# Optimization experiments

Measured on AMD Instinct MI355X. Metric: run time of the kernel, lower is better.

The kernel has to match this reference:

```python
import jax, jax.numpy as jnp
import numpy as np

B, D, L = 8, 512, 8192


def log_g(x):
    # th.where(x >= 0, log(relu(x) + 1), x)
    return jnp.where(x >= 0, jnp.log1p(jnp.maximum(x, 0.0)), x)


def min_gru(hg):
    # hg: [B, H, L] -> [B, H/2, L]
    h, gate = jnp.split(hg, 2, axis=1)
    log_coeffs = -jax.nn.softplus(gate)                      # log a_t
    log_values = -jax.nn.softplus(-gate) + log_g(h)          # log b_t
    a_star = jnp.cumsum(log_coeffs, axis=2)
    log_h0_plus_b_star = jax.lax.cumlogsumexp(log_values - a_star, axis=2)
    return jnp.exp(a_star + log_h0_plus_b_star)


def conv1x1(x, w, b):
    # x: [B, D, L], w: [E, D], b: [E]  (kernel-size-1 Conv1d == pointwise linear)
    return jnp.einsum('ed,bdl->bel', w, x) + b[None, :, None]


def setup_inputs() -> dict:
    key = jax.random.key(0)
    k1, k2, k3, k4, k5 = jax.random.split(key, 5)
    scale = 1.0 / np.sqrt(D)
    x = jax.random.normal(k1, (B, D, L), dtype=jnp.float32)
    w_fore = jax.random.normal(k2, (D, D), dtype=jnp.float32) * scale
    b_fore = jax.random.normal(k3, (D,), dtype=jnp.float32) * scale
    w_back = jax.random.normal(k4, (D, D), dtype=jnp.float32) * scale
    b_back = jax.random.normal(k5, (D,), dtype=jnp.float32) * scale
    return {'x': x, 'w_fore': w_fore, 'b_fore': b_fore, 'w_back': w_back, 'b_back': b_back}


def reference(x, w_fore, b_fore, w_back, b_back):
    fore = min_gru(conv1x1(x, w_fore, b_fore))                            # [B, D/2, L]
    back = jnp.flip(min_gru(conv1x1(jnp.flip(x, 2), w_back, b_back)), 2)  # [B, D/2, L]
    return jnp.concatenate([fore, back], axis=1)                          # [B, D, L]
```

## Files before the change

kernel.cpp:

```cpp
#include <hip/hip_runtime.h>

#define BATCH 8
#define DIN   512
#define SEQ   8192
#define ECH   1024
#define HCH   256
#define CL    32
#define NCHNK (SEQ / CL)
#define NSC   16

typedef __bf16 bf16;
typedef __bf16 bf16x8 __attribute__((ext_vector_type(8)));
typedef float  floatx4 __attribute__((ext_vector_type(4)));

__device__ __forceinline__ void async_ld16(void* lds, const void* g) {
  __builtin_amdgcn_global_load_lds(
      (const __attribute__((address_space(1))) unsigned int*)g,
      (__attribute__((address_space(3))) unsigned int*)lds, 16, 0, 0);
}

__device__ __forceinline__ float bits2f(unsigned u) {
  return __builtin_bit_cast(float, u);
}

__device__ __forceinline__ void gru_ab(unsigned v, float& a, float& bt) {
  float hh = bits2f(v << 16);
  float g  = bits2f(v & 0xffff0000u);
  float eg = __expf(-g);
  float sg = 1.f / (1.f + eg);
  a = eg * sg;
  float gv = hh >= 0.f ? 1.f + hh : __expf(hh);
  bt = sg * gv;
}

__global__ void k_wconv(const float* __restrict__ wf, const float* __restrict__ bfo,
                        const float* __restrict__ wb, const float* __restrict__ bb,
                        bf16* __restrict__ Wf, float* __restrict__ bias) {
  int idx = blockIdx.x * 256 + threadIdx.x;
  if (idx < ECH * DIN) {
    int n = idx >> 9, d = idx & 511;
    int dir = n >> 9, r = n & 511, e = r >> 1, isg = r & 1;
    int s = e + (isg ? HCH : 0);
    const float* w = dir ? wb : wf;
    size_t o = ((size_t)((n >> 4) * 16 + (d >> 5)) << 9) +
               ((((d >> 3) & 3) * 16 + (n & 15)) << 3) + (d & 7);
    Wf[o] = (bf16)w[s * DIN + d];
  }
  if (idx < ECH) {
    int dir = idx >> 9, r = idx & 511, e = r >> 1, isg = r & 1;
    int s = e + (isg ? HCH : 0);
    bias[idx] = (dir ? bb : bfo)[s];
  }
}

__global__ void k_xpose(const float* __restrict__ x, bf16* __restrict__ xT) {
  __shared__ float T[64 * 65];
  int t = threadIdx.x;
  int l0 = blockIdx.x * 64;
  int d0 = blockIdx.y * 64;
  int b  = blockIdx.z;
  const float* xb = x + (size_t)b * DIN * SEQ;
#pragma unroll
  for (int p = 0; p < 4; ++p) {
    int dl = (t >> 4) + p * 16;
    int l4 = (t & 15) * 4;
    float4 v = *(const float4*)(xb + (size_t)(d0 + dl) * SEQ + l0 + l4);
    T[dl * 65 + l4 + 0] = v.x;
    T[dl * 65 + l4 + 1] = v.y;
    T[dl * 65 + l4 + 2] = v.z;
    T[dl * 65 + l4 + 3] = v.w;
  }
  __syncthreads();
  bf16* xTb = xT + (size_t)b * SEQ * DIN;
#pragma unroll
  for (int p = 0; p < 2; ++p) {
    int ll = (t >> 3) + p * 32;
    int d8 = (t & 7) * 8;
    bf16x8 h;
#pragma unroll
    for (int j = 0; j < 8; ++j) h[j] = (bf16)T[(d8 + j) * 65 + ll];
    *(bf16x8*)(xTb + (size_t)(l0 + ll) * DIN + d0 + d8) = h;
  }
}

#define BKK 64
#define NKT (DIN / BKK)

__launch_bounds__(256, 3)
__global__ void k_gemm(const bf16* __restrict__ xT, const bf16* __restrict__ Wf,
                       const float* __restrict__ bias, bf16* __restrict__ hg,
                       float* __restrict__ Asum, float* __restrict__ Bsum) {
  __shared__ __align__(16) bf16 lds[16896];
  bf16* As = lds;

  int t = threadIdx.x;
  int lane = t & 63, wave = t >> 6;
  int l15 = lane & 15, quad = lane >> 4, rsw = l15 & 7;
  int wm = wave >> 1, wn = wave & 1;
  int mb = wm * 64, nb = wn * 64;

  int lin = blockIdx.x + 8 * blockIdx.y;
  int xcd = lin & 7;
  int seq = lin >> 3;
  int ltile = xcd + 8 * (seq >> 3);
  int ntile = seq & 7;
  int n0 = ntile * 128;
  int l0 = ltile * 128;
  int b  = blockIdx.z;

  const bf16* gA = xT + ((size_t)b * SEQ + l0) * DIN;
  int nb16 = (n0 >> 4) + wn * 4;

  float bb4[4];
#pragma unroll
  for (int ni = 0; ni < 4; ++ni) bb4[ni] = bias[n0 + nb + ni * 16 + l15];

  int srow = wave * 32 + (lane >> 3);
  int scol = ((lane & 7) ^ ((lane >> 3) & 7)) * 8;

  floatx4 acc[4][4];
#pragma unroll
  for (int i = 0; i < 4; ++i)
#pragma unroll
    for (int j = 0; j < 4; ++j) acc[i][j] = (floatx4){0.f, 0.f, 0.f, 0.f};

#pragma unroll
  for (int kt = 0; kt < NKT; ++kt) {
    int k0 = kt * BKK;
#pragma unroll
    for (int q = 0; q < 4; ++q)
      async_ld16(As + (wave * 32 + q * 8) * 64,
                 gA + (size_t)(srow + q * 8) * DIN + k0 + scol);

    bf16x8 bfr[4][2];
#pragma unroll
    for (int i = 0; i < 4; ++i)
#pragma unroll
      for (int k2 = 0; k2 < 2; ++k2)
        bfr[i][k2] = *(const bf16x8*)(Wf +
            (((size_t)(nb16 + i) * 16 + kt * 2 + k2) << 9) + lane * 8);

    __syncthreads();

#pragma unroll
    for (int k2 = 0; k2 < 2; ++k2) {
      bf16x8 af[4];
#pragma unroll
      for (int i = 0; i < 4; ++i)
        af[i] = *(const bf16x8*)(As + (mb + i * 16 + l15) * 64 +
                                 (((k2 * 4 + quad) ^ rsw) * 8));
#pragma unroll
      for (int mi = 0; mi < 4; ++mi)
#pragma unroll
        for (int ni = 0; ni < 4; ++ni)
          acc[mi][ni] = __builtin_amdgcn_mfma_f32_16x16x32_bf16(
              af[mi], bfr[ni][k2], acc[mi][ni], 0, 0, 0);
    }
    __syncthreads();
  }

  bf16* Cs = lds;
#pragma unroll
  for (int mi = 0; mi < 4; ++mi)
#pragma unroll
    for (int ni = 0; ni < 4; ++ni)
#pragma unroll
      for (int r = 0; r < 4; ++r) {
        int row = mb + mi * 16 + quad * 4 + r;
        int col = nb + ni * 16 + l15;
        Cs[row * 132 + col] = (bf16)(acc[mi][ni][r] + bb4[ni]);
      }
  __syncthreads();
  bf16* hgb = hg + ((size_t)b * SEQ + l0) * ECH + n0;
#pragma unroll
  for (int p = 0; p < 8; ++p) {
    int row = p * 16 + (t >> 4);
    int seg = t & 15;
    *(bf16x8*)(hgb + (size_t)row * ECH + seg * 8) =
        *(const bf16x8*)(Cs + row * 132 + seg * 8);
  }

  {
    int dirn = ntile >> 2;
    int c = wave, el = lane;
    float A = 1.f, Bc = 0.f;
#pragma unroll 8
    for (int i = 0; i < CL; ++i) {
      int row = c * CL + (dirn ? (CL - 1 - i) : i);
      unsigned v = *(const unsigned*)(Cs + row * 132 + 2 * el);
      float a, bt;
      gru_ab(v, a, bt);
      A *= a;
      Bc = a * Bc + bt;
    }
    int chunkg = ltile * 4 + c;
    int eg = ((n0 & 511) >> 1) + el;
    size_t o = ((size_t)(b * 2 + dirn) * NCHNK + chunkg) * 256 + eg;
    Asum[o] = A;
    Bsum[o] = Bc;
  }
}

__global__ void k_scan2(const float* __restrict__ Asum, const float* __restrict__ Bsum,
                        float* __restrict__ hin) {
  int e = threadIdx.x, row2 = blockIdx.x, dir = row2 & 1;
  size_t base = (size_t)row2 * NCHNK;
  float h = 0.f;
#pragma unroll 8
  for (int i = 0; i < NCHNK; ++i) {
    int c = dir ? (NCHNK - 1 - i) : i;
    size_t o = (base + c) * 256 + e;
    hin[o] = h;
    h = Asum[o] * h + Bsum[o];
  }
}

__global__ void k_scan3(const bf16* __restrict__ hg, const float* __restrict__ hin,
                        float* __restrict__ out) {
  __shared__ float T[256 * 33];
  int t = threadIdx.x;
  int chunk = blockIdx.x, dir = blockIdx.y, b = blockIdx.z;
  const bf16* hb = hg + (size_t)b * SEQ * ECH + dir * 512 + 2 * t;
  float h = hin[((size_t)(b * 2 + dir) * NCHNK + chunk) * 256 + t];
  int lbase = chunk * CL;
#pragma unroll 8
  for (int i = 0; i < CL; ++i) {
    int ll = dir ? (CL - 1 - i) : i;
    unsigned v = *(const unsigned*)(hb + (size_t)(lbase + ll) * ECH);
    float a, bt;
    gru_ab(v, a, bt);
    h = a * h + bt;
    T[t * 33 + ll] = h;
  }
  __syncthreads();
  float* ob = out + ((size_t)b * 512 + dir * 256) * SEQ + lbase;
#pragma unroll
  for (int p = 0; p < 8; ++p) {
    int row = p * 32 + (t >> 3);
    int c4 = (t & 7) * 4;
    float4 v4;
    v4.x = T[row * 33 + c4 + 0];
    v4.y = T[row * 33 + c4 + 1];
    v4.z = T[row * 33 + c4 + 2];
    v4.w = T[row * 33 + c4 + 3];
    *(float4*)(ob + (size_t)row * SEQ + c4) = v4;
  }
}

extern "C" void kernel_launch(void* const* d_in, const int* in_sizes, int n_in,
                              void* d_out, int out_size, void* d_ws, size_t ws_size,
                              hipStream_t stream) {
  const float* x   = (const float*)d_in[0];
  const float* wf  = (const float*)d_in[1];
  const float* bfo = (const float*)d_in[2];
  const float* wb  = (const float*)d_in[3];
  const float* bb  = (const float*)d_in[4];
  float* out = (float*)d_out;
  char* ws = (char*)d_ws;

  bf16*  xT   = (bf16*)(ws);
  bf16*  hg   = (bf16*)(ws + 67108864);
  bf16*  Wfm  = (bf16*)(ws + 201326592);
  float* bias = (float*)(ws + 202375168);
  float* Asum = (float*)(ws + 202379264);
  float* Bsum = (float*)(ws + 206573568);
  float* hin  = (float*)(ws + 210767872);

  k_wconv<<<2048, 256, 0, stream>>>(wf, bfo, wb, bb, Wfm, bias);
  k_xpose<<<dim3(SEQ / 64, DIN / 64, BATCH), 256, 0, stream>>>(x, xT);
  k_gemm<<<dim3(ECH / 128, SEQ / 128, BATCH), 256, 0, stream>>>(xT, Wfm, bias, hg,
                                                                Asum, Bsum);
  k_scan2<<<16, 256, 0, stream>>>(Asum, Bsum, hin);
  k_scan3<<<dim3(NCHNK, 2, BATCH), 256, 0, stream>>>(hg, hin, out);
}
```

Baseline: 382.9 us.

## Store per-step prefix (A,B) pairs from GEMM and split the chunk carry scan hierarchically

The GEMM epilogue now writes packed bf16 prefix products A and prefix affine offsets B for every timestep in place of the raw h/gate tensor, laid out in scan order. The final pass then computes each output as a*h0+b without recomputing exps or running a serial recurrence. The single 16-block serial carry scan over 256 chunks becomes a three-level scan (per-superchunk reduce, 16-step scan, expand) to expose more parallelism. Rounding the prefix products to bf16 loses precision, and the epilogue now issues strided 4-byte global stores per timestep.

```diff
diff --git a/kernel.cpp b/kernel.cpp
--- a/kernel.cpp
+++ b/kernel.cpp
@@ -88,7 +88,7 @@
 
 __launch_bounds__(256, 3)
 __global__ void k_gemm(const bf16* __restrict__ xT, const bf16* __restrict__ Wf,
-                       const float* __restrict__ bias, bf16* __restrict__ hg,
+                       const float* __restrict__ bias, unsigned* __restrict__ P,
                        float* __restrict__ Asum, float* __restrict__ Bsum) {
   __shared__ __align__(16) bf16 lds[16896];
   bf16* As = lds;
@@ -171,66 +171,91 @@
         Cs[row * 132 + col] = (bf16)(acc[mi][ni][r] + bb4[ni]);
       }
   __syncthreads();
-  bf16* hgb = hg + ((size_t)b * SEQ + l0) * ECH + n0;
-#pragma unroll
-  for (int p = 0; p < 8; ++p) {
-    int row = p * 16 + (t >> 4);
-    int seg = t & 15;
-    *(bf16x8*)(hgb + (size_t)row * ECH + seg * 8) =
-        *(const bf16x8*)(Cs + row * 132 + seg * 8);
-  }
 
   {
     int dirn = ntile >> 2;
     int c = wave, el = lane;
+    int chunkg = ltile * 4 + c;
+    int eg = ((n0 & 511) >> 1) + el;
+    int row2 = b * 2 + dirn;
+    unsigned* Pr = P + ((size_t)row2 * SEQ + (size_t)chunkg * CL) * 256 + eg;
     float A = 1.f, Bc = 0.f;
 #pragma unroll 8
     for (int i = 0; i < CL; ++i) {
-      int row = c * CL + (dirn ? (CL - 1 - i) : i);
-      unsigned v = *(const unsigned*)(Cs + row * 132 + 2 * el);
+      int ll = dirn ? (CL - 1 - i) : i;
+      unsigned v = *(const unsigned*)(Cs + (c * CL + ll) * 132 + 2 * el);
       float a, bt;
       gru_ab(v, a, bt);
       A *= a;
       Bc = a * Bc + bt;
+      unsigned lo = (unsigned)__builtin_bit_cast(unsigned short, (bf16)A);
+      unsigned hi = (unsigned)__builtin_bit_cast(unsigned short, (bf16)Bc);
+      Pr[(size_t)ll * 256] = (hi << 16) | lo;
     }
-    int chunkg = ltile * 4 + c;
-    int eg = ((n0 & 511) >> 1) + el;
-    size_t o = ((size_t)(b * 2 + dirn) * NCHNK + chunkg) * 256 + eg;
+    size_t o = ((size_t)row2 * NCHNK + chunkg) * 256 + eg;
     Asum[o] = A;
     Bsum[o] = Bc;
   }
 }
 
-__global__ void k_scan2(const float* __restrict__ Asum, const float* __restrict__ Bsum,
-                        float* __restrict__ hin) {
+__global__ void k_scan2a(const float* __restrict__ Asum, const float* __restrict__ Bsum,
+                         float* __restrict__ SA, float* __restrict__ SB) {
+  int e = threadIdx.x, sc = blockIdx.x, row2 = blockIdx.y, dir = row2 & 1;
+  size_t base = (size_t)row2 * NCHNK;
+  float Acc = 1.f, Bcc = 0.f;
+#pragma unroll
+  for (int i = 0; i < 16; ++i) {
+    int c = sc * 16 + (dir ? 15 - i : i);
+    size_t o = (base + c) * 256 + e;
+    float a = Asum[o], bv = Bsum[o];
+    Acc = a * Acc;
+    Bcc = a * Bcc + bv;
+  }
+  size_t so = ((size_t)row2 * NSC + sc) * 256 + e;
+  SA[so] = Acc;
+  SB[so] = Bcc;
+}
+
+__global__ void k_scan2b(const float* __restrict__ SA, const float* __restrict__ SB,
+                         float* __restrict__ hsc) {
   int e = threadIdx.x, row2 = blockIdx.x, dir = row2 & 1;
-  size_t base = (size_t)row2 * NCHNK;
   float h = 0.f;
-#pragma unroll 8
-  for (int i = 0; i < NCHNK; ++i) {
-    int c = dir ? (NCHNK - 1 - i) : i;
-    size_t o = (base + c) * 256 + e;
+  for (int i = 0; i < NSC; ++i) {
+    int sc = dir ? NSC - 1 - i : i;
+    size_t o = ((size_t)row2 * NSC + sc) * 256 + e;
+    hsc[o] = h;
+    h = SA[o] * h + SB[o];
+  }
+}
+
+__global__ void k_scan2c(const float* __restrict__ Asum, const float* __restrict__ Bsum,
+                         const float* __restrict__ hsc, float* __restrict__ hin) {
+  int e = threadIdx.x, sc = blockIdx.x, row2 = blockIdx.y, dir = row2 & 1;
+  float h = hsc[((size_t)row2 * NSC + sc) * 256 + e];
+#pragma unroll
+  for (int i = 0; i < 16; ++i) {
+    int c = sc * 16 + (dir ? 15 - i : i);
+    size_t o = ((size_t)row2 * NCHNK + c) * 256 + e;
     hin[o] = h;
     h = Asum[o] * h + Bsum[o];
   }
 }
 
-__global__ void k_scan3(const bf16* __restrict__ hg, const float* __restrict__ hin,
+__global__ void k_scan3(const unsigned* __restrict__ P, const float* __restrict__ hin,
                         float* __restrict__ out) {
   __shared__ float T[256 * 33];
   int t = threadIdx.x;
   int chunk = blockIdx.x, dir = blockIdx.y, b = blockIdx.z;
-  const bf16* hb = hg + (size_t)b * SEQ * ECH + dir * 512 + 2 * t;
-  float h = hin[((size_t)(b * 2 + dir) * NCHNK + chunk) * 256 + t];
+  int row2 = b * 2 + dir;
+  const unsigned* Pb = P + ((size_t)row2 * SEQ + (size_t)chunk * CL) * 256 + t;
+  float h0 = hin[((size_t)row2 * NCHNK + chunk) * 256 + t];
   int lbase = chunk * CL;
-#pragma unroll 8
-  for (int i = 0; i < CL; ++i) {
-    int ll = dir ? (CL - 1 - i) : i;
-    unsigned v = *(const unsigned*)(hb + (size_t)(lbase + ll) * ECH);
-    float a, bt;
-    gru_ab(v, a, bt);
-    h = a * h + bt;
-    T[t * 33 + ll] = h;
+#pragma unroll
+  for (int ll = 0; ll < CL; ++ll) {
+    unsigned v = Pb[(size_t)ll * 256];
+    float a  = bits2f(v << 16);
+    float bt = bits2f(v & 0xffff0000u);
+    T[t * 33 + ll] = a * h0 + bt;
   }
   __syncthreads();
   float* ob = out + ((size_t)b * 512 + dir * 256) * SEQ + lbase;
@@ -258,18 +283,23 @@
   float* out = (float*)d_out;
   char* ws = (char*)d_ws;
 
-  bf16*  xT   = (bf16*)(ws);
-  bf16*  hg   = (bf16*)(ws + 67108864);
-  bf16*  Wfm  = (bf16*)(ws + 201326592);
-  float* bias = (float*)(ws + 202375168);
-  float* Asum = (float*)(ws + 202379264);
-  float* Bsum = (float*)(ws + 206573568);
-  float* hin  = (float*)(ws + 210767872);
+  bf16*     xT   = (bf16*)(ws);
+  unsigned* P    = (unsigned*)(ws + 67108864);
+  bf16*     Wfm  = (bf16*)(ws + 201326592);
+  float*    bias = (float*)(ws + 202375168);
+  float*    Asum = (float*)(ws + 202379264);
+  float*    Bsum = (float*)(ws + 206573568);
+  float*    hin  = (float*)(ws + 210767872);
+  float*    SA   = (float*)(ws + 214962176);
+  float*    SB   = (float*)(ws + 215224320);
+  float*    hsc  = (float*)(ws + 215486464);
 
   k_wconv<<<2048, 256, 0, stream>>>(wf, bfo, wb, bb, Wfm, bias);
   k_xpose<<<dim3(SEQ / 64, DIN / 64, BATCH), 256, 0, stream>>>(x, xT);
-  k_gemm<<<dim3(ECH / 128, SEQ / 128, BATCH), 256, 0, stream>>>(xT, Wfm, bias, hg,
+  k_gemm<<<dim3(ECH / 128, SEQ / 128, BATCH), 256, 0, stream>>>(xT, Wfm, bias, P,
                                                                 Asum, Bsum);
-  k_scan2<<<16, 256, 0, stream>>>(Asum, Bsum, hin);
-  k_scan3<<<dim3(NCHNK, 2, BATCH), 256, 0, stream>>>(hg, hin, out);
-}
+  k_scan2a<<<dim3(NSC, 16), 256, 0, stream>>>(Asum, Bsum, SA, SB);
+  k_scan2b<<<16, 256, 0, stream>>>(SA, SB, hsc);
+  k_scan2c<<<dim3(NSC, 16), 256, 0, stream>>>(Asum, Bsum, hsc, hin);
+  k_scan3<<<dim3(NCHNK, 2, BATCH), 256, 0, stream>>>(P, hin, out);
+}
```

After: 382.2 us. About the same (-0.2%).

## Split serial chunk-carry scan into three-level hierarchical scan; widen scan3 loads

Applied to the files above, without the earlier changes.

The single 16-block serial scan over 256 chunk carries is replaced by a three-stage hierarchy. The first stage reduces groups of 16 chunks in parallel, the second scans the 16 super-chunks, and the third propagates carries back into the per-chunk values. This cuts the long dependent chain that ran on very few blocks, at the cost of two extra kernel launches and some extra global traffic. Separately, in scan3 each thread now handles two channels with 8-byte loads, so only half the threads do the recurrence.

```diff
diff --git a/kernel.cpp b/kernel.cpp
--- a/kernel.cpp
+++ b/kernel.cpp
@@ -201,15 +201,44 @@
   }
 }
 
-__global__ void k_scan2(const float* __restrict__ Asum, const float* __restrict__ Bsum,
-                        float* __restrict__ hin) {
+__global__ void k_scan2a(const float* __restrict__ Asum, const float* __restrict__ Bsum,
+                         float* __restrict__ SA, float* __restrict__ SB) {
+  int e = threadIdx.x, sc = blockIdx.x, row2 = blockIdx.y, dir = row2 & 1;
+  size_t base = (size_t)row2 * NCHNK;
+  float Acc = 1.f, Bcc = 0.f;
+#pragma unroll
+  for (int i = 0; i < 16; ++i) {
+    int c = sc * 16 + (dir ? 15 - i : i);
+    size_t o = (base + c) * 256 + e;
+    float a = Asum[o], bv = Bsum[o];
+    Acc = a * Acc;
+    Bcc = a * Bcc + bv;
+  }
+  size_t so = ((size_t)row2 * NSC + sc) * 256 + e;
+  SA[so] = Acc;
+  SB[so] = Bcc;
+}
+
+__global__ void k_scan2b(const float* __restrict__ SA, const float* __restrict__ SB,
+                         float* __restrict__ hsc) {
   int e = threadIdx.x, row2 = blockIdx.x, dir = row2 & 1;
-  size_t base = (size_t)row2 * NCHNK;
   float h = 0.f;
-#pragma unroll 8
-  for (int i = 0; i < NCHNK; ++i) {
-    int c = dir ? (NCHNK - 1 - i) : i;
-    size_t o = (base + c) * 256 + e;
+  for (int i = 0; i < NSC; ++i) {
+    int sc = dir ? NSC - 1 - i : i;
+    size_t o = ((size_t)row2 * NSC + sc) * 256 + e;
+    hsc[o] = h;
+    h = SA[o] * h + SB[o];
+  }
+}
+
+__global__ void k_scan2c(const float* __restrict__ Asum, const float* __restrict__ Bsum,
+                         const float* __restrict__ hsc, float* __restrict__ hin) {
+  int e = threadIdx.x, sc = blockIdx.x, row2 = blockIdx.y, dir = row2 & 1;
+  float h = hsc[((size_t)row2 * NSC + sc) * 256 + e];
+#pragma unroll
+  for (int i = 0; i < 16; ++i) {
+    int c = sc * 16 + (dir ? 15 - i : i);
+    size_t o = ((size_t)row2 * NCHNK + c) * 256 + e;
     hin[o] = h;
     h = Asum[o] * h + Bsum[o];
   }
@@ -220,17 +249,26 @@
   __shared__ float T[256 * 33];
   int t = threadIdx.x;
   int chunk = blockIdx.x, dir = blockIdx.y, b = blockIdx.z;
-  const bf16* hb = hg + (size_t)b * SEQ * ECH + dir * 512 + 2 * t;
-  float h = hin[((size_t)(b * 2 + dir) * NCHNK + chunk) * 256 + t];
+  int row2 = b * 2 + dir;
   int lbase = chunk * CL;
+  if (t < 128) {
+    int J = t;
+    const bf16* hb = hg + (size_t)(b * SEQ + lbase) * ECH + dir * 512 + 4 * J;
+    const float* hb0 = hin + ((size_t)row2 * NCHNK + chunk) * 256 + 2 * J;
+    float h0 = hb0[0];
+    float h1 = hb0[1];
 #pragma unroll 8
-  for (int i = 0; i < CL; ++i) {
-    int ll = dir ? (CL - 1 - i) : i;
-    unsigned v = *(const unsigned*)(hb + (size_t)(lbase + ll) * ECH);
-    float a, bt;
-    gru_ab(v, a, bt);
-    h = a * h + bt;
-    T[t * 33 + ll] = h;
+    for (int i = 0; i < CL; ++i) {
+      int ll = dir ? (CL - 1 - i) : i;
+      uint2 v2 = *(const uint2*)(hb + (size_t)ll * ECH);
+      float a0, b0v, a1, b1v;
+      gru_ab(v2.x, a0, b0v);
+      gru_ab(v2.y, a1, b1v);
+      h0 = a0 * h0 + b0v;
+      h1 = a1 * h1 + b1v;
+      T[(2 * J + 0) * 33 + ll] = h0;
+      T[(2 * J + 1) * 33 + ll] = h1;
+    }
   }
   __syncthreads();
   float* ob = out + ((size_t)b * 512 + dir * 256) * SEQ + lbase;
@@ -265,11 +303,16 @@
   float* Asum = (float*)(ws + 202379264);
   float* Bsum = (float*)(ws + 206573568);
   float* hin  = (float*)(ws + 210767872);
+  float* SA   = (float*)(ws + 214962176);
+  float* SB   = (float*)(ws + 215224320);
+  float* hsc  = (float*)(ws + 215486464);
 
   k_wconv<<<2048, 256, 0, stream>>>(wf, bfo, wb, bb, Wfm, bias);
   k_xpose<<<dim3(SEQ / 64, DIN / 64, BATCH), 256, 0, stream>>>(x, xT);
   k_gemm<<<dim3(ECH / 128, SEQ / 128, BATCH), 256, 0, stream>>>(xT, Wfm, bias, hg,
                                                                 Asum, Bsum);
-  k_scan2<<<16, 256, 0, stream>>>(Asum, Bsum, hin);
+  k_scan2a<<<dim3(NSC, 16), 256, 0, stream>>>(Asum, Bsum, SA, SB);
+  k_scan2b<<<16, 256, 0, stream>>>(SA, SB, hsc);
+  k_scan2c<<<dim3(NSC, 16), 256, 0, stream>>>(Asum, Bsum, hsc, hin);
   k_scan3<<<dim3(NCHNK, 2, BATCH), 256, 0, stream>>>(hg, hin, out);
 }
```

After: 376.0 us. About the same (-1.8%).
